# Kernel optimization log

Measured on AMD Instinct MI355X. Metric: run time of the kernel, lower is better.

The kernel has to match this reference:

```python
import jax, jax.numpy as jnp
import numpy as np

FP8_MAX = 448.0  # max normal for float8_e4m3fn
BLOCK = 128


def setup_inputs() -> dict:
    key = jax.random.key(0)
    k1, k2, k3 = jax.random.split(key, 3)
    B, S, D_IN, D_OUT = 2, 2048, 4096, 8192
    x = jax.random.normal(k1, (B, S, D_IN), dtype=jnp.float32)
    # stored weight is fp8_e4m3fn; materialize as f32 values that are exactly fp8-representable
    w = jax.random.normal(k2, (D_OUT, D_IN), dtype=jnp.float32)
    weight = w.astype(jnp.float8_e4m3fn).astype(jnp.float32)
    # positive per-(128x128)-block dequant scales
    weight_scale_inv = (
        jax.random.uniform(k3, (D_OUT // BLOCK, D_IN // BLOCK), dtype=jnp.float32) * 0.05 + 0.005
    )
    return {"x": x, "weight": weight, "weight_scale_inv": weight_scale_inv}


def _quantize_per_token(x2d):
    # x2d: [M, K] -> fp8 values + [M, 1] f32 scale
    amax = jnp.clip(jnp.max(jnp.abs(x2d), axis=-1, keepdims=True), min=1e-12)
    x_scale = (amax / FP8_MAX).astype(jnp.float32)
    x_fp8 = (x2d / x_scale).astype(jnp.float8_e4m3fn)
    return x_fp8, x_scale


def _dequantize_weight(weight, weight_scale_inv):
    # weight: [O, K] (fp8-representable f32), scales: [O/B, K/B]
    O, K = weight.shape
    w_fp8 = weight.astype(jnp.float8_e4m3fn).astype(jnp.float32)
    wb = w_fp8.reshape(O // BLOCK, BLOCK, K // BLOCK, BLOCK)
    wb = wb * weight_scale_inv[:, None, :, None]
    return wb.reshape(O, K)


def reference(x, weight, weight_scale_inv):
    orig_shape = x.shape
    x2d = x.reshape(-1, orig_shape[-1])  # [M, K], M > 1 path
    x_fp8, x_scale = _quantize_per_token(x2d)
    # block-scaled fp8 GEMM: y[m,n] = x_scale[m] * sum_k x_fp8[m,k] * w_fp8[n,k] * s[n//B,k//B]
    w_deq = _dequantize_weight(weight, weight_scale_inv)  # [O, K]
    y = jnp.einsum("mk,ok->mo", x_fp8.astype(jnp.float32), w_deq) * x_scale
    return y.reshape(*orig_shape[:-1], weight.shape[0])
```

## Files before the change

### kernel.cpp

```cpp
#include <hip/hip_runtime.h>

typedef float f32x4  __attribute__((ext_vector_type(4)));
typedef float f32x16 __attribute__((ext_vector_type(16)));
typedef int   i32x4  __attribute__((ext_vector_type(4)));
typedef int   i32x8  __attribute__((ext_vector_type(8)));

#define AS1 __attribute__((address_space(1)))
#define AS3 __attribute__((address_space(3)))

__global__ __launch_bounds__(256) void quant_x_fp8_kernel(
    const float* __restrict__ x, unsigned char* __restrict__ x8,
    float* __restrict__ xs, int K) {
  int m = blockIdx.x;
  int t = threadIdx.x;
  const f32x4* src = (const f32x4*)(x + (size_t)m * K + t * 16);
  f32x4 v[4];
  float am = 0.0f;
#pragma unroll
  for (int i = 0; i < 4; ++i) {
    v[i] = src[i];
#pragma unroll
    for (int j = 0; j < 4; ++j) am = fmaxf(am, __builtin_fabsf(v[i][j]));
  }
#pragma unroll
  for (int off = 32; off >= 1; off >>= 1)
    am = fmaxf(am, __shfl_xor(am, off, 64));
  __shared__ float red[4];
  int wv = t >> 6, lane = t & 63;
  if (lane == 0) red[wv] = am;
  __syncthreads();
  am = fmaxf(fmaxf(red[0], red[1]), fmaxf(red[2], red[3]));
  am = fmaxf(am, 1e-12f);
  float sc = am / 448.0f;
  if (t == 0) xs[m] = sc;
  i32x4 out;
#pragma unroll
  for (int i = 0; i < 4; ++i) {
    float q0 = v[i][0] / sc, q1 = v[i][1] / sc;
    float q2 = v[i][2] / sc, q3 = v[i][3] / sc;
    int p = __builtin_amdgcn_cvt_pk_fp8_f32(q0, q1, 0, false);
    p = __builtin_amdgcn_cvt_pk_fp8_f32(q2, q3, p, true);
    out[i] = p;
  }
  *(i32x4*)(x8 + (size_t)m * K + t * 16) = out;
}

__global__ __launch_bounds__(256) void quant_w_fp8_kernel(
    const float* __restrict__ w, unsigned char* __restrict__ w8) {
  size_t idx = (size_t)blockIdx.x * 256 + threadIdx.x;
  const f32x4* src = (const f32x4*)w + idx * 4;
  i32x4 out;
#pragma unroll
  for (int i = 0; i < 4; ++i) {
    f32x4 v = src[i];
    int p = __builtin_amdgcn_cvt_pk_fp8_f32(v[0], v[1], 0, false);
    p = __builtin_amdgcn_cvt_pk_fp8_f32(v[2], v[3], p, true);
    out[i] = p;
  }
  ((i32x4*)w8)[idx] = out;
}

__global__ __launch_bounds__(512, 1) void gemm_mxfp8_kernel(
    const unsigned char* __restrict__ A8,
    const unsigned char* __restrict__ W8,
    const float* __restrict__ xs,
    const float* __restrict__ wsinv,
    float* __restrict__ Y,
    int M, int N, int K) {
  const int KB = K >> 7;

  int bid = blockIdx.x, nwg = gridDim.x;
  int wg = (bid & 7) * (nwg >> 3) + (bid >> 3);
  int mt = M >> 8;
  int bm = wg & (mt - 1);
  int bn = wg / mt;
  int m0 = bm << 8, n0 = bn << 7;

  __shared__ __align__(16) char lds[81920];

  const int tid = threadIdx.x, wv = tid >> 6, lane = tid & 63;
  const int wr = wv >> 1, wc = wv & 1;
  const int l31 = lane & 31, hi2 = lane >> 5;
  const int salt = l31 & 7;

  const int sL0 = ((hi2 * 2 + 0) ^ salt) << 4;
  const int sH0 = ((hi2 * 2 + 1) ^ salt) << 4;
  const int sL1 = ((4 + hi2 * 2 + 0) ^ salt) << 4;
  const int sH1 = ((4 + hi2 * 2 + 1) ^ salt) << 4;

  const int aRow = (wr * 64 + l31) * 128;
  const int bRow = (wc * 64 + l31) * 128;
  const int aL0 = aRow + sL0, aH0 = aRow + sH0;
  const int aL1 = aRow + sL1, aH1 = aRow + sH1;
  const int bL0 = bRow + sL0, bH0 = bRow + sH0;
  const int bL1 = bRow + sL1, bH1 = bRow + sH1;

  const int stgD = tid << 4;
  const int rIdx = tid >> 3;
  const int cSrc = ((tid & 7) ^ ((tid >> 3) & 7)) << 4;
  const size_t rowB = (size_t)K;
  const size_t g64 = 64 * rowB;
  const char* pA = (const char*)A8 + (size_t)(m0 + rIdx) * rowB + cSrc;
  const char* pB = (const char*)W8 + (size_t)(n0 + rIdx) * rowB + cSrc;

  const float* wsv = wsinv + (size_t)bn * KB;

  f32x16 acc[2][2];
#pragma unroll
  for (int i = 0; i < 2; ++i)
#pragma unroll
    for (int j = 0; j < 2; ++j) acc[i][j] = (f32x16)0.0f;

  i32x8 af[2], bf[2][2];

#define GL(SRC, DST)                                                           \
  __builtin_amdgcn_global_load_lds((const AS1 void*)(SRC), (AS3 void*)(DST),   \
                                   16, 0, 0)
#define STG_A(COND, SB, SRC)                                                   \
  if (COND) {                                                                  \
    const char* s_ = (SRC);                                                    \
    char* d_ = lds + (SB) + stgD;                                              \
    GL(s_, d_);                                                                \
    GL(s_ + g64, d_ + 8192);                                                   \
    GL(s_ + 2 * g64, d_ + 16384);                                              \
    GL(s_ + 3 * g64, d_ + 24576);                                              \
  }
#define STG_B(COND, SB, SRC)                                                   \
  if (COND) {                                                                  \
    const char* s_ = (SRC);                                                    \
    char* d_ = lds + (SB) + stgD;                                              \
    GL(s_, d_);                                                                \
    GL(s_ + g64, d_ + 8192);                                                   \
  }

#define RD_A(RB, MJ)                                                           \
  {                                                                            \
    const char* p_ = lds + (RB) + (MJ) * 4096;                                 \
    i32x4 lo0 = *(const i32x4*)(p_ + aL0);                                     \
    i32x4 hi0 = *(const i32x4*)(p_ + aH0);                                     \
    i32x4 lo1 = *(const i32x4*)(p_ + aL1);                                     \
    i32x4 hi1 = *(const i32x4*)(p_ + aH1);                                     \
    af[0] = __builtin_shufflevector(lo0, hi0, 0, 1, 2, 3, 4, 5, 6, 7);         \
    af[1] = __builtin_shufflevector(lo1, hi1, 0, 1, 2, 3, 4, 5, 6, 7);         \
  }
#define RD_B(BR)                                                               \
  _Pragma("unroll") for (int nj = 0; nj < 2; ++nj) {                           \
    const char* p_ = lds + (BR) + nj * 4096;                                   \
    i32x4 lo0 = *(const i32x4*)(p_ + bL0);                                     \
    i32x4 hi0 = *(const i32x4*)(p_ + bH0);                                     \
    i32x4 lo1 = *(const i32x4*)(p_ + bL1);                                     \
    i32x4 hi1 = *(const i32x4*)(p_ + bH1);                                     \
    bf[nj][0] = __builtin_shufflevector(lo0, hi0, 0, 1, 2, 3, 4, 5, 6, 7);     \
    bf[nj][1] = __builtin_shufflevector(lo1, hi1, 0, 1, 2, 3, 4, 5, 6, 7);     \
  }

#define MMFn(MJ, NJ, R_)                                                       \
  {                                                                            \
    _Pragma("unroll") for (int q = 0; q < 16; ++q)                             \
        acc[MJ][NJ][q] *= (R_);                                                \
    acc[MJ][NJ] = __builtin_amdgcn_mfma_scale_f32_32x32x64_f8f6f4(             \
        af[0], bf[NJ][0], acc[MJ][NJ], 0, 0, 0, 0x7f7f7f7f, 0, 0x7f7f7f7f);    \
    acc[MJ][NJ] = __builtin_amdgcn_mfma_scale_f32_32x32x64_f8f6f4(             \
        af[1], bf[NJ][1], acc[MJ][NJ], 0, 0, 0, 0x7f7f7f7f, 0, 0x7f7f7f7f);    \
  }

  STG_A(true, 0, pA);
  STG_B(true, 65536, pB);
  asm volatile("s_waitcnt vmcnt(0)" ::: "memory");
  __builtin_amdgcn_s_barrier();

  int rdA = 0, stA = 32768;
  const char* pAs = pA + 128;
  const char* pBs = pB + 128;
  float sp_ = wsv[0];

#define TILE(T, G)                                                             \
  {                                                                            \
    float sc_ = wsv[(T)];                                                      \
    float r_ = sp_ / sc_;                                                      \
    RD_B(65536);                                                               \
    RD_A(rdA, 0);                                                              \
    STG_A(G, stA, pAs);                                                        \
    __builtin_amdgcn_s_setprio(1);                                             \
    MMFn(0, 0, r_);                                                            \
    __builtin_amdgcn_s_setprio(0);                                             \
    asm volatile("s_waitcnt lgkmcnt(0)" ::: "memory");                         \
    __builtin_amdgcn_s_barrier();                                              \
    STG_B(G, 65536, pBs);                                                      \
    __builtin_amdgcn_s_setprio(1);                                             \
    MMFn(0, 1, r_);                                                            \
    __builtin_amdgcn_s_setprio(0);                                             \
    RD_A(rdA, 1);                                                              \
    __builtin_amdgcn_s_setprio(1);                                             \
    MMFn(1, 0, r_);                                                            \
    MMFn(1, 1, r_);                                                            \
    __builtin_amdgcn_s_setprio(0);                                             \
    sp_ = sc_;                                                                 \
    asm volatile("s_waitcnt vmcnt(0)" ::: "memory");                           \
    __builtin_amdgcn_s_barrier();                                              \
    rdA ^= 32768;                                                              \
    stA ^= 32768;                                                              \
    pAs += 128;                                                                \
    pBs += 128;                                                                \
  }

#pragma unroll 1
  for (int t = 0; t < KB - 1; ++t) {
    TILE(t, true)
  }
  TILE(KB - 1, false)

#undef TILE
#undef MMFn
#undef RD_B
#undef RD_A
#undef STG_B
#undef STG_A
#undef GL

  const float sl_ = sp_;
#pragma unroll
  for (int mj = 0; mj < 2; ++mj)
#pragma unroll
    for (int nj = 0; nj < 2; ++nj) {
      int col = n0 + wc * 64 + nj * 32 + l31;
#pragma unroll
      for (int q = 0; q < 4; ++q) {
        int row0 = m0 + wr * 64 + mj * 32 + q * 8 + hi2 * 4;
        f32x4 sv = *(const f32x4*)(xs + row0);
#pragma unroll
        for (int j = 0; j < 4; ++j)
          Y[(size_t)(row0 + j) * N + col] = acc[mj][nj][q * 4 + j] * sv[j] * sl_;
      }
    }
}

extern "C" void kernel_launch(void* const* d_in, const int* in_sizes, int n_in,
                              void* d_out, int out_size, void* d_ws, size_t ws_size,
                              hipStream_t stream) {
  const float* x     = (const float*)d_in[0];
  const float* w     = (const float*)d_in[1];
  const float* wsinv = (const float*)d_in[2];
  float* y = (float*)d_out;

  const int K = 4096;
  const int M = in_sizes[0] / K;
  const int N = in_sizes[1] / K;

  unsigned char* x8 = (unsigned char*)d_ws;
  float* xs = (float*)((char*)d_ws + (size_t)M * K);
  unsigned char* w8 =
      (unsigned char*)d_ws + (size_t)M * K + (size_t)M * 4;

  quant_x_fp8_kernel<<<M, 256, 0, stream>>>(x, x8, xs, K);
  quant_w_fp8_kernel<<<(int)(((size_t)N * K / 16 + 255) / 256), 256, 0,
                       stream>>>(w, w8);

  dim3 grid((M / 256) * (N / 128));
  gemm_mxfp8_kernel<<<grid, 512, 0, stream>>>(x8, w8, xs, wsinv, y, M, N, K);
}
```

Measured before the change: 238.9 us.

## Shrink GEMM tile to 128x128 with 256 threads and full A/B double buffering

Changes the GEMM workgroup from 512 threads on a 256x128 tile to 256 threads on a 128x128 tile. The tile loop is restructured so both A and B are double-buffered in 64KB of LDS, which removes the mid-tile barrier and lgkmcnt wait. Launch bounds now ask for two workgroups per CU, aiming to overlap loads from one workgroup with MFMA work from the other. The trade-off is twice as many workgroups and lower operand reuse per tile, so more global and L2 traffic.

```diff
diff --git a/kernel.cpp b/kernel.cpp
--- a/kernel.cpp
+++ b/kernel.cpp
@@ -60,7 +60,7 @@
   ((i32x4*)w8)[idx] = out;
 }
 
-__global__ __launch_bounds__(512, 1) void gemm_mxfp8_kernel(
+__global__ __launch_bounds__(256, 2) void gemm_mxfp8_kernel(
     const unsigned char* __restrict__ A8,
     const unsigned char* __restrict__ W8,
     const float* __restrict__ xs,
@@ -71,12 +71,12 @@
 
   int bid = blockIdx.x, nwg = gridDim.x;
   int wg = (bid & 7) * (nwg >> 3) + (bid >> 3);
-  int mt = M >> 8;
+  int mt = M >> 7;
   int bm = wg & (mt - 1);
   int bn = wg / mt;
-  int m0 = bm << 8, n0 = bn << 7;
-
-  __shared__ __align__(16) char lds[81920];
+  int m0 = bm << 7, n0 = bn << 7;
+
+  __shared__ __align__(16) char lds[65536];
 
   const int tid = threadIdx.x, wv = tid >> 6, lane = tid & 63;
   const int wr = wv >> 1, wc = wv & 1;
@@ -99,7 +99,7 @@
   const int rIdx = tid >> 3;
   const int cSrc = ((tid & 7) ^ ((tid >> 3) & 7)) << 4;
   const size_t rowB = (size_t)K;
-  const size_t g64 = 64 * rowB;
+  const size_t g32 = 32 * rowB;
   const char* pA = (const char*)A8 + (size_t)(m0 + rIdx) * rowB + cSrc;
   const char* pB = (const char*)W8 + (size_t)(n0 + rIdx) * rowB + cSrc;
 
@@ -116,21 +116,14 @@
 #define GL(SRC, DST)                                                           \
   __builtin_amdgcn_global_load_lds((const AS1 void*)(SRC), (AS3 void*)(DST),   \
                                    16, 0, 0)
-#define STG_A(COND, SB, SRC)                                                   \
+#define STG(COND, SB, SRC)                                                     \
   if (COND) {                                                                  \
     const char* s_ = (SRC);                                                    \
     char* d_ = lds + (SB) + stgD;                                              \
     GL(s_, d_);                                                                \
-    GL(s_ + g64, d_ + 8192);                                                   \
-    GL(s_ + 2 * g64, d_ + 16384);                                              \
-    GL(s_ + 3 * g64, d_ + 24576);                                              \
-  }
-#define STG_B(COND, SB, SRC)                                                   \
-  if (COND) {                                                                  \
-    const char* s_ = (SRC);                                                    \
-    char* d_ = lds + (SB) + stgD;                                              \
-    GL(s_, d_);                                                                \
-    GL(s_ + g64, d_ + 8192);                                                   \
+    GL(s_ + g32, d_ + 4096);                                                   \
+    GL(s_ + 2 * g32, d_ + 8192);                                               \
+    GL(s_ + 3 * g32, d_ + 12288);                                              \
   }
 
 #define RD_A(RB, MJ)                                                           \
@@ -143,9 +136,9 @@
     af[0] = __builtin_shufflevector(lo0, hi0, 0, 1, 2, 3, 4, 5, 6, 7);         \
     af[1] = __builtin_shufflevector(lo1, hi1, 0, 1, 2, 3, 4, 5, 6, 7);         \
   }
-#define RD_B(BR)                                                               \
+#define RD_B(RB)                                                               \
   _Pragma("unroll") for (int nj = 0; nj < 2; ++nj) {                           \
-    const char* p_ = lds + (BR) + nj * 4096;                                   \
+    const char* p_ = lds + (RB) + 16384 + nj * 4096;                           \
     i32x4 lo0 = *(const i32x4*)(p_ + bL0);                                     \
     i32x4 hi0 = *(const i32x4*)(p_ + bH0);                                     \
     i32x4 lo1 = *(const i32x4*)(p_ + bL1);                                     \
@@ -164,33 +157,28 @@
         af[1], bf[NJ][1], acc[MJ][NJ], 0, 0, 0, 0x7f7f7f7f, 0, 0x7f7f7f7f);    \
   }
 
-  STG_A(true, 0, pA);
-  STG_B(true, 65536, pB);
+  STG(true, 0, pA);
+  STG(true, 16384, pB);
   asm volatile("s_waitcnt vmcnt(0)" ::: "memory");
   __builtin_amdgcn_s_barrier();
 
-  int rdA = 0, stA = 32768;
   const char* pAs = pA + 128;
   const char* pBs = pB + 128;
   float sp_ = wsv[0];
 
-#define TILE(T, G)                                                             \
+#define TILE(T, RB, SB, G)                                                     \
   {                                                                            \
     float sc_ = wsv[(T)];                                                      \
     float r_ = sp_ / sc_;                                                      \
-    RD_B(65536);                                                               \
-    RD_A(rdA, 0);                                                              \
-    STG_A(G, stA, pAs);                                                        \
+    RD_B(RB);                                                                  \
+    RD_A(RB, 0);                                                               \
+    STG(G, (SB), pAs);                                                         \
+    STG(G, (SB) + 16384, pBs);                                                 \
     __builtin_amdgcn_s_setprio(1);                                             \
     MMFn(0, 0, r_);                                                            \
-    __builtin_amdgcn_s_setprio(0);                                             \
-    asm volatile("s_waitcnt lgkmcnt(0)" ::: "memory");                         \
-    __builtin_amdgcn_s_barrier();                                              \
-    STG_B(G, 65536, pBs);                                                      \
-    __builtin_amdgcn_s_setprio(1);                                             \
     MMFn(0, 1, r_);                                                            \
     __builtin_amdgcn_s_setprio(0);                                             \
-    RD_A(rdA, 1);                                                              \
+    RD_A(RB, 1);                                                               \
     __builtin_amdgcn_s_setprio(1);                                             \
     MMFn(1, 0, r_);                                                            \
     MMFn(1, 1, r_);                                                            \
@@ -198,24 +186,21 @@
     sp_ = sc_;                                                                 \
     asm volatile("s_waitcnt vmcnt(0)" ::: "memory");                           \
     __builtin_amdgcn_s_barrier();                                              \
-    rdA ^= 32768;                                                              \
-    stA ^= 32768;                                                              \
     pAs += 128;                                                                \
     pBs += 128;                                                                \
   }
 
 #pragma unroll 1
-  for (int t = 0; t < KB - 1; ++t) {
-    TILE(t, true)
-  }
-  TILE(KB - 1, false)
+  for (int t = 0; t < KB; t += 2) {
+    TILE(t, 0, 32768, true)
+    TILE(t + 1, 32768, 0, (t + 2) < KB)
+  }
 
 #undef TILE
 #undef MMFn
 #undef RD_B
 #undef RD_A
-#undef STG_B
-#undef STG_A
+#undef STG
 #undef GL
 
   const float sl_ = sp_;
@@ -256,6 +241,6 @@
   quant_w_fp8_kernel<<<(int)(((size_t)N * K / 16 + 255) / 256), 256, 0,
                        stream>>>(w, w8);
 
-  dim3 grid((M / 256) * (N / 128));
-  gemm_mxfp8_kernel<<<grid, 512, 0, stream>>>(x8, w8, xs, wsinv, y, M, N, K);
-}
+  dim3 grid((M / 128) * (N / 128));
+  gemm_mxfp8_kernel<<<grid, 256, 0, stream>>>(x8, w8, xs, wsinv, y, M, N, K);
+}
```

Measured after the change: 219.6 us. 1.09x faster.
